# Kernel tuning notes

Hardware: AMD Instinct MI355X
Metric: run time of the kernel (lower is better)

The kernel has to match this reference:

```python
import jax, jax.numpy as jnp
import numpy as np

D = 128   # node feature dim
C = 2     # classes
N = 50000 # nodes
E = 500000  # edges (before self-loops)
H1 = 2    # conv1 heads
NEG_SLOPE = 0.2
BN_EPS = 1e-5


def setup_inputs() -> dict:
    key = jax.random.key(0)
    ks = jax.random.split(key, 24)
    rn = lambda k, shape, s=0.05: jax.random.normal(k, shape, dtype=jnp.float32) * s
    inp = {
        'x': jax.random.normal(ks[0], (N, D), dtype=jnp.float32),
        'edge_index': jax.random.randint(ks[1], (2, E), 0, N, dtype=jnp.int64),
        # conv1: GATConv(D, D, heads=2, concat=True)
        'W1': rn(ks[2], (D, H1 * D)),
        'att_src1': rn(ks[3], (H1, D)),
        'att_dst1': rn(ks[4], (H1, D)),
        'bias1': jnp.zeros((H1 * D,), jnp.float32),
        # conv2: GATConv(2D, D, heads=1, concat=False)
        'W2': rn(ks[5], (2 * D, D)),
        'att_src2': rn(ks[6], (1, D)),
        'att_dst2': rn(ks[7], (1, D)),
        'bias2': jnp.zeros((D,), jnp.float32),
        # lin1 = MLP([3D, 96]) : Linear -> ReLU -> BatchNorm1d
        'Wl': rn(ks[8], (3 * D, 96)), 'bl': jnp.zeros((96,), jnp.float32),
        'gl': jnp.ones((96,), jnp.float32), 'betal': jnp.zeros((96,), jnp.float32),
        # mlp1 = MLP([96, 96, C]) : two (Linear -> ReLU -> BN) blocks
        'Wa': rn(ks[9], (96, 96)), 'ba': jnp.zeros((96,), jnp.float32),
        'ga': jnp.ones((96,), jnp.float32), 'betaa': jnp.zeros((96,), jnp.float32),
        'Wb': rn(ks[10], (96, C)), 'bb': jnp.zeros((C,), jnp.float32),
        'gb': jnp.ones((C,), jnp.float32), 'betab': jnp.zeros((C,), jnp.float32),
    }
    return inp


def gat_conv(x, src, dst, W, att_src, att_dst, bias, heads, out_dim, concat):
    # PyG GATConv: h = x W -> [N,H,F]; per-edge logit leakyrelu(a_s.h_src + a_d.h_dst);
    # segment softmax over edges grouped by destination; weighted scatter-sum.
    n = x.shape[0]
    h = (x @ W).reshape(n, heads, out_dim)
    a_src = jnp.einsum('nhd,hd->nh', h, att_src)  # [N,H]
    a_dst = jnp.einsum('nhd,hd->nh', h, att_dst)
    alpha = jax.nn.leaky_relu(a_src[src] + a_dst[dst], NEG_SLOPE)  # [Etot,H]
    m = jax.ops.segment_max(alpha, dst, num_segments=n)            # [N,H]
    e = jnp.exp(alpha - m[dst])
    s = jax.ops.segment_sum(e, dst, num_segments=n)
    w = e / (s[dst] + 1e-16)                                       # [Etot,H]
    out = jax.ops.segment_sum(h[src] * w[:, :, None], dst, num_segments=n)  # [N,H,F]
    out = out.reshape(n, heads * out_dim) if concat else out.mean(axis=1)
    return out + bias


def mlp_block(x, W, b, gamma, beta):
    # Linear -> ReLU -> BatchNorm1d (training-mode batch stats, biased var)
    y = jax.nn.relu(x @ W + b)
    mu = y.mean(axis=0)
    var = ((y - mu) ** 2).mean(axis=0)
    return gamma * (y - mu) / jnp.sqrt(var + BN_EPS) + beta


def reference(x, edge_index, W1, att_src1, att_dst1, bias1,
              W2, att_src2, att_dst2, bias2,
              Wl, bl, gl, betal, Wa, ba, ga, betaa, Wb, bb, gb, betab):
    n = x.shape[0]
    # PyG GATConv default add_self_loops=True
    loops = jnp.arange(n, dtype=edge_index.dtype)
    src = jnp.concatenate([edge_index[0], loops])
    dst = jnp.concatenate([edge_index[1], loops])
    x1 = gat_conv(x, src, dst, W1, att_src1, att_dst1, bias1, H1, D, True)    # [N,2D]
    x2 = gat_conv(x1, src, dst, W2, att_src2, att_dst2, bias2, 1, D, False)   # [N,D]
    h = jnp.concatenate([x1, x2], axis=1)                                      # [N,3D]
    h = mlp_block(h, Wl, bl, gl, betal)     # lin1
    h = mlp_block(h, Wa, ba, ga, betaa)     # mlp1 layer 1
    h = mlp_block(h, Wb, bb, gb, betab)     # mlp1 layer 2
    return h
```

## Files before the change

kernel.cpp:

```cpp
#include <hip/hip_runtime.h>
#include <hip/hip_bf16.h>
#include <cstdint>
#include <cstddef>

#define NNODES 50000
#define NEDGES 500000
#define ETOT   (NEDGES + NNODES)

typedef __attribute__((ext_vector_type(8))) short short8;
typedef __attribute__((ext_vector_type(8))) unsigned short ushort8v;
typedef __attribute__((ext_vector_type(4))) float floatx4;
typedef __attribute__((ext_vector_type(4))) unsigned short ushort4v;

__device__ __forceinline__ unsigned short f2bf(float f) {
    union { __hip_bfloat16 h; unsigned short u; } cv;
    cv.h = __float2bfloat16(f);
    return cv.u;
}
__device__ __forceinline__ float bf2f(unsigned short u) {
    union { unsigned int i; float f; } cv;
    cv.i = ((unsigned int)u) << 16;
    return cv.f;
}

#define GBM 128
#define GBN 64
#define GBK 32

__global__ __launch_bounds__(256, 4) void gemm_mfma(
    const unsigned short* __restrict__ A, int lda,
    const unsigned short* __restrict__ Bt,
    float* __restrict__ C,
    unsigned short* __restrict__ Cb, int ldc,
    const float* __restrict__ bias,
    float* __restrict__ colsum, float* __restrict__ colsq,
    const float* __restrict__ att_s, const float* __restrict__ att_d,
    float* __restrict__ as_out, float* __restrict__ ad_out, int Hheads,
    int M, int N, int K, int do_relu)
{
    __shared__ __attribute__((aligned(16))) unsigned short Alds[GBM * GBK];
    __shared__ __attribute__((aligned(16))) unsigned short Blds[GBN * GBK];
    __shared__ float scol[GBN], sqcol[GBN];

    int tid = threadIdx.x;
    int wave = tid >> 6, lane = tid & 63;
    int row0 = blockIdx.y * GBM;
    int col0 = blockIdx.x * GBN;
    int m = lane & 15, q = lane >> 4;

    floatx4 acc[2][4] = {};

    for (int k0 = 0; k0 < K; k0 += GBK) {
        #pragma unroll
        for (int i = 0; i < 2; ++i) {
            int c = tid + i * 256;
            int r = c >> 2, off = (c & 3) * 8;
            int gr = row0 + r;
            short8 v = {};
            if (gr < M) v = *(const short8*)(A + (size_t)gr * lda + k0 + off);
            *(short8*)(Alds + r * GBK + off) = v;
        }
        {
            int r = tid >> 2, off = (tid & 3) * 8;
            short8 v = *(const short8*)(Bt + (size_t)(col0 + r) * K + k0 + off);
            *(short8*)(Blds + r * GBK + off) = v;
        }
        __syncthreads();

        short8 a0 = *(const short8*)(Alds + (wave * 32 + m) * GBK + q * 8);
        short8 a1 = *(const short8*)(Alds + (wave * 32 + 16 + m) * GBK + q * 8);
        #pragma unroll
        for (int ct = 0; ct < 4; ++ct) {
            short8 b = *(const short8*)(Blds + (ct * 16 + m) * GBK + q * 8);
            acc[0][ct] = __builtin_amdgcn_mfma_f32_16x16x32_bf16(a0, b, acc[0][ct], 0, 0, 0);
            acc[1][ct] = __builtin_amdgcn_mfma_f32_16x16x32_bf16(a1, b, acc[1][ct], 0, 0, 0);
        }
        __syncthreads();
    }

    float ps[4] = {}, pq[4] = {};
    #pragma unroll
    for (int rt = 0; rt < 2; ++rt) {
        #pragma unroll
        for (int r = 0; r < 4; ++r) {
            int gr = row0 + wave * 32 + rt * 16 + q * 4 + r;
            float ds = 0.f, dd = 0.f;
            #pragma unroll
            for (int ct = 0; ct < 4; ++ct) {
                int gc = col0 + ct * 16 + m;
                float v = acc[rt][ct][r];
                if (gc < N) {
                    float vb = v;
                    if (bias != nullptr) vb += bias[gc];
                    if (do_relu) vb = fmaxf(vb, 0.f);
                    if (att_s != nullptr) { ds += vb * att_s[gc]; dd += vb * att_d[gc]; }
                    if (gr < M) {
                        if (C  != nullptr) C[(size_t)gr * ldc + gc] = vb;
                        if (Cb != nullptr) Cb[(size_t)gr * ldc + gc] = f2bf(vb);
                        ps[ct] += vb; pq[ct] += vb * vb;
                    }
                }
            }
            if (att_s != nullptr) {
                #pragma unroll
                for (int off = 1; off < 16; off <<= 1) {
                    ds += __shfl_xor(ds, off);
                    dd += __shfl_xor(dd, off);
                }
                if (m == 0 && gr < M) {
                    int head = col0 >> 7;
                    atomicAdd(&as_out[gr * Hheads + head], ds);
                    atomicAdd(&ad_out[gr * Hheads + head], dd);
                }
            }
        }
    }
    if (colsum != nullptr) {
        if (tid < GBN) { scol[tid] = 0.f; sqcol[tid] = 0.f; }
        __syncthreads();
        #pragma unroll
        for (int ct = 0; ct < 4; ++ct) {
            atomicAdd(&scol[ct * 16 + m], ps[ct]);
            atomicAdd(&sqcol[ct * 16 + m], pq[ct]);
        }
        __syncthreads();
        if (tid < GBN) {
            int gc = col0 + tid;
            if (gc < N) {
                atomicAdd(&colsum[gc], scol[tid]);
                atomicAdd(&colsq[gc], sqcol[tid]);
            }
        }
    }
}

__global__ __launch_bounds__(256) void fold_att(
    const float* __restrict__ W1, const float* __restrict__ as1v, const float* __restrict__ ad1v,
    const float* __restrict__ W2, const float* __restrict__ as2v, const float* __restrict__ ad2v,
    float* __restrict__ U1, float* __restrict__ U2)
{
    int g = threadIdx.x >> 5, l = threadIdx.x & 31;
    int task = blockIdx.x * 8 + g;
    float ss = 0.f, sd = 0.f;
    if (task < 256) {
        int d = task & 127, h = task >> 7;
        const float4 wv = *(const float4*)(W1 + d * 256 + h * 128 + l * 4);
        const float4 av = *(const float4*)(as1v + h * 128 + l * 4);
        const float4 bv = *(const float4*)(ad1v + h * 128 + l * 4);
        ss = wv.x * av.x + wv.y * av.y + wv.z * av.z + wv.w * av.w;
        sd = wv.x * bv.x + wv.y * bv.y + wv.z * bv.z + wv.w * bv.w;
    } else {
        int k = task - 256;
        const float4 wv = *(const float4*)(W2 + (size_t)k * 128 + l * 4);
        const float4 av = *(const float4*)(as2v + l * 4);
        const float4 bv = *(const float4*)(ad2v + l * 4);
        ss = wv.x * av.x + wv.y * av.y + wv.z * av.z + wv.w * av.w;
        sd = wv.x * bv.x + wv.y * bv.y + wv.z * bv.z + wv.w * bv.w;
    }
    #pragma unroll
    for (int off = 1; off < 32; off <<= 1) { ss += __shfl_xor(ss, off); sd += __shfl_xor(sd, off); }
    if (l == 0) {
        if (task < 256) {
            int d = task & 127, h = task >> 7;
            U1[h * 128 + d] = ss;
            U1[256 + h * 128 + d] = sd;
        } else {
            int k = task - 256;
            U2[k] = ss;
            U2[256 + k] = sd;
        }
    }
}

__global__ __launch_bounds__(256) void cast_x_att(
    const float* __restrict__ x, const float* __restrict__ U1,
    unsigned short* __restrict__ xb, float* __restrict__ as1, float* __restrict__ ad1)
{
    __shared__ float Us[512];
    int tid = threadIdx.x;
    Us[tid] = U1[tid];
    Us[tid + 256] = U1[tid + 256];
    __syncthreads();
    int g = tid >> 5, l = tid & 31;
    int n = blockIdx.x * 8 + g;
    if (n >= NNODES) return;
    const float4 v = *(const float4*)(x + (size_t)n * 128 + l * 4);
    ushort4v o;
    o.x = f2bf(v.x); o.y = f2bf(v.y); o.z = f2bf(v.z); o.w = f2bf(v.w);
    *(ushort4v*)(xb + (size_t)n * 128 + l * 4) = o;
    const float4 us0 = *(const float4*)(Us + l * 4);
    const float4 us1 = *(const float4*)(Us + 128 + l * 4);
    const float4 ud0 = *(const float4*)(Us + 256 + l * 4);
    const float4 ud1 = *(const float4*)(Us + 384 + l * 4);
    float s0 = v.x * us0.x + v.y * us0.y + v.z * us0.z + v.w * us0.w;
    float s1 = v.x * us1.x + v.y * us1.y + v.z * us1.z + v.w * us1.w;
    float d0 = v.x * ud0.x + v.y * ud0.y + v.z * ud0.z + v.w * ud0.w;
    float d1 = v.x * ud1.x + v.y * ud1.y + v.z * ud1.z + v.w * ud1.w;
    #pragma unroll
    for (int off = 1; off < 32; off <<= 1) {
        s0 += __shfl_xor(s0, off); s1 += __shfl_xor(s1, off);
        d0 += __shfl_xor(d0, off); d1 += __shfl_xor(d1, off);
    }
    if (l == 0) {
        as1[n * 2] = s0; as1[n * 2 + 1] = s1;
        ad1[n * 2] = d0; ad1[n * 2 + 1] = d1;
    }
}

__global__ void cast_weights(const float* __restrict__ W1, const float* __restrict__ W2,
                             const float* __restrict__ Wl,
                             unsigned short* __restrict__ W1t, unsigned short* __restrict__ W2t,
                             unsigned short* __restrict__ Wlt) {
    int i = blockIdx.x * 256 + threadIdx.x;
    if (i < 32768) {
        int n = i >> 7, k = i & 127;
        W1t[i] = f2bf(W1[k * 256 + n]);
    } else if (i < 65536) {
        int j = i - 32768;
        int n = j >> 8, k = j & 255;
        W2t[j] = f2bf(W2[k * 128 + n]);
    } else if (i < 114688) {
        int j = i - 65536;
        int n = j / 384, k = j % 384;
        Wlt[j] = (n < 96) ? f2bf(Wl[(size_t)k * 96 + n]) : (unsigned short)0;
    }
}

__global__ void bnfold_a(const float* __restrict__ csum, const float* __restrict__ csq,
                         const float* __restrict__ gamma, const float* __restrict__ beta,
                         const float* __restrict__ Wa, const float* __restrict__ ba,
                         unsigned short* __restrict__ Wat2, float* __restrict__ ba_f) {
    __shared__ float scl[96], shf[96];
    int tid = threadIdx.x;
    if (tid < 96) {
        float mu  = csum[tid] / (float)NNODES;
        float var = csq[tid] / (float)NNODES - mu * mu;
        if (var < 0.f) var = 0.f;
        float sc = gamma[tid] * rsqrtf(var + 1e-5f);
        scl[tid] = sc; shf[tid] = beta[tid] - mu * sc;
    }
    __syncthreads();
    for (int idx = tid; idx < 128 * 96; idx += 256) {
        int n = idx / 96, k = idx % 96;
        Wat2[idx] = (n < 96) ? f2bf(scl[k] * Wa[k * 96 + n]) : (unsigned short)0;
    }
    if (tid < 96) {
        float s = ba[tid];
        for (int k = 0; k < 96; ++k) s += shf[k] * Wa[k * 96 + tid];
        ba_f[tid] = s;
    }
}

__global__ void bnfold_b(const float* __restrict__ csum, const float* __restrict__ csq,
                         const float* __restrict__ gamma, const float* __restrict__ beta,
                         const float* __restrict__ Wb, const float* __restrict__ bb,
                         unsigned short* __restrict__ Wbt, float* __restrict__ bb_f) {
    __shared__ float scl[96], shf[96];
    int tid = threadIdx.x;
    if (tid < 96) {
        float mu  = csum[tid] / (float)NNODES;
        float var = csq[tid] / (float)NNODES - mu * mu;
        if (var < 0.f) var = 0.f;
        float sc = gamma[tid] * rsqrtf(var + 1e-5f);
        scl[tid] = sc; shf[tid] = beta[tid] - mu * sc;
    }
    __syncthreads();
    for (int idx = tid; idx < 64 * 96; idx += 256) {
        int n = idx / 96, k = idx % 96;
        Wbt[idx] = (n < 2) ? f2bf(scl[k] * Wb[k * 2 + n]) : (unsigned short)0;
    }
    if (tid < 2) {
        float s = bb[tid];
        for (int k = 0; k < 96; ++k) s += shf[k] * Wb[k * 2 + tid];
        bb_f[tid] = s;
    }
}

__global__ void bn_fin_apply(const float* __restrict__ csum, const float* __restrict__ csq,
                             const float* __restrict__ gamma, const float* __restrict__ beta,
                             float* __restrict__ y, int total) {
    int i = blockIdx.x * blockDim.x + threadIdx.x;
    if (i >= total) return;
    int j = i & 1;
    float mu  = csum[j] / (float)NNODES;
    float var = csq[j] / (float)NNODES - mu * mu;
    if (var < 0.f) var = 0.f;
    float sc = gamma[j] * rsqrtf(var + 1e-5f);
    float sh = beta[j] - mu * sc;
    y[i] = y[i] * sc + sh;
}

__device__ __forceinline__ void edge_src_dst(const int* ei, int e, int& src, int& dst) {
    if (e < NEDGES) { src = ei[e]; dst = ei[NEDGES + e]; }
    else { src = e - NEDGES; dst = src; }
}

__global__ __launch_bounds__(256) void csr_count(const int* __restrict__ ei, int* __restrict__ cnt) {
    int e = blockIdx.x * blockDim.x + threadIdx.x;
    if (e >= ETOT) return;
    int src, dst; edge_src_dst(ei, e, src, dst); (void)src;
    atomicAdd(&cnt[dst], 1);
}

#define SCAN_CH 1024
#define SCAN_NB ((NNODES + SCAN_CH - 1) / SCAN_CH)

__global__ __launch_bounds__(256) void scan1(const int* __restrict__ cnt, int* __restrict__ part) {
    int t = threadIdx.x;
    int base = blockIdx.x * SCAN_CH + t * 4;
    int4 v = {0, 0, 0, 0};
    if (base + 3 < NNODES) v = *(const int4*)(cnt + base);
    else {
        if (base + 0 < NNODES) v.x = cnt[base + 0];
        if (base + 1 < NNODES) v.y = cnt[base + 1];
        if (base + 2 < NNODES) v.z = cnt[base + 2];
        if (base + 3 < NNODES) v.w = cnt[base + 3];
    }
    int s = v.x + v.y + v.z + v.w;
    __shared__ int sm[256];
    sm[t] = s;
    __syncthreads();
    for (int off = 128; off > 0; off >>= 1) {
        if (t < off) sm[t] += sm[t + off];
        __syncthreads();
    }
    if (t == 0) part[blockIdx.x] = sm[0];
}

__global__ void scan2(int* __restrict__ part, int* __restrict__ rowstart) {
    int lane = threadIdx.x;
    int v = (lane < SCAN_NB) ? part[lane] : 0;
    #pragma unroll
    for (int off = 1; off < 64; off <<= 1) {
        int t = __shfl_up(v, off);
        if (lane >= off) v += t;
    }
    int ex = __shfl_up(v, 1);
    if (lane == 0) ex = 0;
    if (lane < SCAN_NB) part[lane] = ex;
    if (lane == 0) rowstart[NNODES] = ETOT;
}

__global__ __launch_bounds__(256) void scan3(const int* __restrict__ cnt, const int* __restrict__ part,
                                             int* __restrict__ rowstart, int* __restrict__ cursor) {
    int t = threadIdx.x;
    int base = blockIdx.x * SCAN_CH + t * 4;
    int4 v = {0, 0, 0, 0};
    if (base + 3 < NNODES) v = *(const int4*)(cnt + base);
    else {
        if (base + 0 < NNODES) v.x = cnt[base + 0];
        if (base + 1 < NNODES) v.y = cnt[base + 1];
        if (base + 2 < NNODES) v.z = cnt[base + 2];
        if (base + 3 < NNODES) v.w = cnt[base + 3];
    }
    int s = v.x + v.y + v.z + v.w;
    __shared__ int sm[2][256];
    sm[0][t] = s;
    __syncthreads();
    int cur = 0;
    #pragma unroll
    for (int off = 1; off < 256; off <<= 1) {
        int nxt = cur ^ 1;
        int val = sm[cur][t];
        if (t >= off) val += sm[cur][t - off];
        sm[nxt][t] = val;
        __syncthreads();
        cur = nxt;
    }
    int p = sm[cur][t] - s + part[blockIdx.x];
    if (base + 0 < NNODES) { rowstart[base + 0] = p; cursor[base + 0] = p; } p += v.x;
    if (base + 1 < NNODES) { rowstart[base + 1] = p; cursor[base + 1] = p; } p += v.y;
    if (base + 2 < NNODES) { rowstart[base + 2] = p; cursor[base + 2] = p; } p += v.z;
    if (base + 3 < NNODES) { rowstart[base + 3] = p; cursor[base + 3] = p; }
}

__global__ __launch_bounds__(256) void csr_fill(const int* __restrict__ ei,
                                                int* __restrict__ cursor,
                                                int* __restrict__ esrc) {
    int e = blockIdx.x * blockDim.x + threadIdx.x;
    if (e >= ETOT) return;
    int src, dst; edge_src_dst(ei, e, src, dst);
    int pos = atomicAdd(&cursor[dst], 1);
    esrc[pos] = src;
}

__global__ __launch_bounds__(256) void gat_gather_x2(
    const int* __restrict__ rowstart, const int* __restrict__ esrc,
    const unsigned short* __restrict__ xb, const float* __restrict__ a_src,
    const float* __restrict__ a_dst, unsigned short* __restrict__ xaggh)
{
    int tid = threadIdx.x;
    int t = tid & 15;
    int g0 = (blockIdx.x * blockDim.x + tid) >> 4;
    int gstride = (gridDim.x * blockDim.x) >> 4;

    for (int n = g0; n < NNODES; n += gstride) {
        int beg = rowstart[n], deg = rowstart[n + 1] - beg;
        const float2 adv = *(const float2*)(a_dst + (size_t)n * 2);
        float acc0[8] = {}, acc1[8] = {};

        if (deg <= 32) {
            int sa = 0, sb = 0;
            float la0 = -1e30f, la1 = -1e30f;
            float lb0 = -1e30f, lb1 = -1e30f;
            if (t < deg) {
                sa = esrc[beg + t];
                const float2 asv = *(const float2*)(a_src + (size_t)sa * 2);
                la0 = asv.x + adv.x; la0 = la0 >= 0.f ? la0 : 0.2f * la0;
                lb0 = asv.y + adv.y; lb0 = lb0 >= 0.f ? lb0 : 0.2f * lb0;
            }
            if (t + 16 < deg) {
                sb = esrc[beg + 16 + t];
                const float2 asv = *(const float2*)(a_src + (size_t)sb * 2);
                la1 = asv.x + adv.x; la1 = la1 >= 0.f ? la1 : 0.2f * la1;
                lb1 = asv.y + adv.y; lb1 = lb1 >= 0.f ? lb1 : 0.2f * lb1;
            }
            float m0 = fmaxf(la0, la1), m1 = fmaxf(lb0, lb1);
            #pragma unroll
            for (int off = 1; off < 16; off <<= 1) {
                m0 = fmaxf(m0, __shfl_xor(m0, off, 16));
                m1 = fmaxf(m1, __shfl_xor(m1, off, 16));
            }
            float ea0 = (t < deg)      ? __expf(la0 - m0) : 0.f;
            float ea1 = (t + 16 < deg) ? __expf(la1 - m0) : 0.f;
            float eb0 = (t < deg)      ? __expf(lb0 - m1) : 0.f;
            float eb1 = (t + 16 < deg) ? __expf(lb1 - m1) : 0.f;
            float s0 = ea0 + ea1, s1 = eb0 + eb1;
            #pragma unroll
            for (int off = 1; off < 16; off <<= 1) {
                s0 += __shfl_xor(s0, off, 16);
                s1 += __shfl_xor(s1, off, 16);
            }
            float i0 = 1.f / (s0 + 1e-16f), i1 = 1.f / (s1 + 1e-16f);
            float wa0 = ea0 * i0, wa1 = ea1 * i0;
            float wb0 = eb0 * i1, wb1 = eb1 * i1;

            int e = 0;
            for (; e + 3 < deg; e += 4) {
                int sx[4]; float w0x[4], w1x[4];
                #pragma unroll
                for (int u = 0; u < 4; ++u) {
                    int ee = e + u;
                    int hi = ee & 16, ln = ee & 15;
                    sx[u]  = __shfl(hi ? sb  : sa,  ln, 16);
                    w0x[u] = __shfl(hi ? wa1 : wa0, ln, 16);
                    w1x[u] = __shfl(hi ? wb1 : wb0, ln, 16);
                }
                ushort8v hv[4];
                #pragma unroll
                for (int u = 0; u < 4; ++u)
                    hv[u] = *(const ushort8v*)(xb + (size_t)sx[u] * 128 + t * 8);
                #pragma unroll
                for (int u = 0; u < 4; ++u) {
                    #pragma unroll
                    for (int j = 0; j < 8; ++j) {
                        float f = bf2f(hv[u][j]);
                        acc0[j] += w0x[u] * f;
                        acc1[j] += w1x[u] * f;
                    }
                }
            }
            for (; e < deg; ++e) {
                int hi = e & 16, ln = e & 15;
                int   sX  = __shfl(hi ? sb  : sa,  ln, 16);
                float wX0 = __shfl(hi ? wa1 : wa0, ln, 16);
                float wX1 = __shfl(hi ? wb1 : wb0, ln, 16);
                const ushort8v hv = *(const ushort8v*)(xb + (size_t)sX * 128 + t * 8);
                #pragma unroll
                for (int j = 0; j < 8; ++j) {
                    float f = bf2f(hv[j]);
                    acc0[j] += wX0 * f; acc1[j] += wX1 * f;
                }
            }
        } else {
            float m0 = -1e30f, m1 = -1e30f;
            for (int idx = t; idx < deg; idx += 16) {
                int s = esrc[beg + idx];
                const float2 asv = *(const float2*)(a_src + (size_t)s * 2);
                float l0 = asv.x + adv.x; l0 = l0 >= 0.f ? l0 : 0.2f * l0;
                float l1 = asv.y + adv.y; l1 = l1 >= 0.f ? l1 : 0.2f * l1;
                m0 = fmaxf(m0, l0); m1 = fmaxf(m1, l1);
            }
            #pragma unroll
            for (int off = 1; off < 16; off <<= 1) {
                m0 = fmaxf(m0, __shfl_xor(m0, off, 16));
                m1 = fmaxf(m1, __shfl_xor(m1, off, 16));
            }
            float s0 = 0.f, s1 = 0.f;
            for (int idx = t; idx < deg; idx += 16) {
                int s = esrc[beg + idx];
                const float2 asv = *(const float2*)(a_src + (size_t)s * 2);
                float l0 = asv.x + adv.x; l0 = l0 >= 0.f ? l0 : 0.2f * l0;
                float l1 = asv.y + adv.y; l1 = l1 >= 0.f ? l1 : 0.2f * l1;
                s0 += __expf(l0 - m0); s1 += __expf(l1 - m1);
            }
            #pragma unroll
            for (int off = 1; off < 16; off <<= 1) {
                s0 += __shfl_xor(s0, off, 16);
                s1 += __shfl_xor(s1, off, 16);
            }
            float inv0 = 1.f / (s0 + 1e-16f), inv1 = 1.f / (s1 + 1e-16f);
            for (int e = 0; e < deg; ++e) {
                int s = esrc[beg + e];
                const float2 asv = *(const float2*)(a_src + (size_t)s * 2);
                float l0 = asv.x + adv.x; l0 = l0 >= 0.f ? l0 : 0.2f * l0;
                float l1 = asv.y + adv.y; l1 = l1 >= 0.f ? l1 : 0.2f * l1;
                float w0 = __expf(l0 - m0) * inv0, w1 = __expf(l1 - m1) * inv1;
                const ushort8v hv = *(const ushort8v*)(xb + (size_t)s * 128 + t * 8);
                #pragma unroll
                for (int j = 0; j < 8; ++j) {
                    float f = bf2f(hv[j]);
                    acc0[j] += w0 * f; acc1[j] += w1 * f;
                }
            }
        }

        ushort8v o0, o1;
        #pragma unroll
        for (int j = 0; j < 8; ++j) { o0[j] = f2bf(acc0[j]); o1[j] = f2bf(acc1[j]); }
        *(ushort8v*)(xaggh + (size_t)n * 256 + t * 8) = o0;
        *(ushort8v*)(xaggh + (size_t)n * 256 + 128 + t * 8) = o1;
    }
}

__global__ __launch_bounds__(256) void gat_gather_h1(
    const int* __restrict__ rowstart, const int* __restrict__ esrc,
    const unsigned short* __restrict__ hb, const float* __restrict__ a_src,
    const float* __restrict__ a_dst, const float* __restrict__ bias,
    unsigned short* __restrict__ xcat)
{
    int tid = threadIdx.x;
    int t = tid & 15;
    int g0 = (blockIdx.x * blockDim.x + tid) >> 4;
    int gstride = (gridDim.x * blockDim.x) >> 4;

    for (int n = g0; n < NNODES; n += gstride) {
        int beg = rowstart[n], deg = rowstart[n + 1] - beg;
        float ad0 = a_dst[n];
        float acc[8] = {};

        if (deg <= 32) {
            int sa = 0, sb = 0;
            float l0 = -1e30f, l1 = -1e30f;
            if (t < deg) {
                sa = esrc[beg + t];
                l0 = a_src[sa] + ad0; l0 = l0 >= 0.f ? l0 : 0.2f * l0;
            }
            if (t + 16 < deg) {
                sb = esrc[beg + 16 + t];
                l1 = a_src[sb] + ad0; l1 = l1 >= 0.f ? l1 : 0.2f * l1;
            }
            float m0 = fmaxf(l0, l1);
            #pragma unroll
            for (int off = 1; off < 16; off <<= 1)
                m0 = fmaxf(m0, __shfl_xor(m0, off, 16));
            float e0 = (t < deg)      ? __expf(l0 - m0) : 0.f;
            float e1 = (t + 16 < deg) ? __expf(l1 - m0) : 0.f;
            float s0 = e0 + e1;
            #pragma unroll
            for (int off = 1; off < 16; off <<= 1)
                s0 += __shfl_xor(s0, off, 16);
            float i0 = 1.f / (s0 + 1e-16f);
            float w0 = e0 * i0, w1 = e1 * i0;

            int e = 0;
            for (; e + 3 < deg; e += 4) {
                int sx[4]; float wx[4];
                #pragma unroll
                for (int u = 0; u < 4; ++u) {
                    int ee = e + u;
                    int hi = ee & 16, ln = ee & 15;
                    sx[u] = __shfl(hi ? sb : sa, ln, 16);
                    wx[u] = __shfl(hi ? w1 : w0, ln, 16);
                }
                ushort8v hv[4];
                #pragma unroll
                for (int u = 0; u < 4; ++u)
                    hv[u] = *(const ushort8v*)(hb + (size_t)sx[u] * 128 + t * 8);
                #pragma unroll
                for (int u = 0; u < 4; ++u) {
                    #pragma unroll
                    for (int j = 0; j < 8; ++j)
                        acc[j] += wx[u] * bf2f(hv[u][j]);
                }
            }
            for (; e < deg; ++e) {
                int hi = e & 16, ln = e & 15;
                int   sX = __shfl(hi ? sb : sa, ln, 16);
                float wX = __shfl(hi ? w1 : w0, ln, 16);
                const ushort8v hv = *(const ushort8v*)(hb + (size_t)sX * 128 + t * 8);
                #pragma unroll
                for (int j = 0; j < 8; ++j) acc[j] += wX * bf2f(hv[j]);
            }
        } else {
            float m0 = -1e30f;
            for (int idx = t; idx < deg; idx += 16) {
                int s = esrc[beg + idx];
                float l = a_src[s] + ad0; l = l >= 0.f ? l : 0.2f * l;
                m0 = fmaxf(m0, l);
            }
            #pragma unroll
            for (int off = 1; off < 16; off <<= 1)
                m0 = fmaxf(m0, __shfl_xor(m0, off, 16));
            float s0 = 0.f;
            for (int idx = t; idx < deg; idx += 16) {
                int s = esrc[beg + idx];
                float l = a_src[s] + ad0; l = l >= 0.f ? l : 0.2f * l;
                s0 += __expf(l - m0);
            }
            #pragma unroll
            for (int off = 1; off < 16; off <<= 1)
                s0 += __shfl_xor(s0, off, 16);
            float inv0 = 1.f / (s0 + 1e-16f);
            for (int e = 0; e < deg; ++e) {
                int s = esrc[beg + e];
                float l = a_src[s] + ad0; l = l >= 0.f ? l : 0.2f * l;
                float w = __expf(l - m0) * inv0;
                const ushort8v hv = *(const ushort8v*)(hb + (size_t)s * 128 + t * 8);
                #pragma unroll
                for (int j = 0; j < 8; ++j) acc[j] += w * bf2f(hv[j]);
            }
        }

        const float4 b0 = *(const float4*)(bias + t * 8);
        const float4 b1 = *(const float4*)(bias + t * 8 + 4);
        ushort8v o;
        o[0] = f2bf(acc[0] + b0.x); o[1] = f2bf(acc[1] + b0.y);
        o[2] = f2bf(acc[2] + b0.z); o[3] = f2bf(acc[3] + b0.w);
        o[4] = f2bf(acc[4] + b1.x); o[5] = f2bf(acc[5] + b1.y);
        o[6] = f2bf(acc[6] + b1.z); o[7] = f2bf(acc[7] + b1.w);
        *(ushort8v*)(xcat + (size_t)n * 384 + 256 + t * 8) = o;
    }
}

extern "C" void kernel_launch(void* const* d_in, const int* in_sizes, int n_in,
                              void* d_out, int out_size, void* d_ws, size_t ws_size,
                              hipStream_t stream) {
    const float* x        = (const float*)d_in[0];
    const int*   ei       = (const int*)d_in[1];
    const float* W1       = (const float*)d_in[2];
    const float* att_src1 = (const float*)d_in[3];
    const float* att_dst1 = (const float*)d_in[4];
    const float* bias1    = (const float*)d_in[5];
    const float* W2       = (const float*)d_in[6];
    const float* att_src2 = (const float*)d_in[7];
    const float* att_dst2 = (const float*)d_in[8];
    const float* bias2    = (const float*)d_in[9];
    const float* Wl       = (const float*)d_in[10];
    const float* bl       = (const float*)d_in[11];
    const float* gl       = (const float*)d_in[12];
    const float* betal    = (const float*)d_in[13];
    const float* Wa       = (const float*)d_in[14];
    const float* ba       = (const float*)d_in[15];
    const float* ga       = (const float*)d_in[16];
    const float* betaa    = (const float*)d_in[17];
    const float* Wb       = (const float*)d_in[18];
    const float* bb       = (const float*)d_in[19];
    const float* gb       = (const float*)d_in[20];
    const float* betab    = (const float*)d_in[21];
    float* out = (float*)d_out;
    char* ws = (char*)d_ws;

    const int N = NNODES;

    const size_t offY2b  = 0;
    const size_t offXcat = 19200000;
    const size_t offXb   = 57600000;
    const size_t offY1b  = 70400000;
    const size_t offXagg = 80000000;
    const size_t offW1t  = 105600000;
    const size_t offW2t  = 105665536;
    const size_t offWlt  = 105731072;
    const size_t offWat2 = 105829376;
    const size_t offWbt  = 105853952;
    const size_t offBaf  = 105866240;
    const size_t offBbf  = 105866640;
    const size_t offU1   = 105867264;
    const size_t offU2   = 105869312;
    const size_t offRow  = 106000000;
    const size_t offCur  = 106200128;
    const size_t offEsrc = 106400832;
    const size_t offPart = 108700000;
    const size_t offAs1  = 108800000;
    const size_t offAd1  = 109200000;
    const size_t offAs2  = 109600000;
    const size_t offAd2  = 109800000;
    const size_t offSt   = 110000000;

    unsigned short* y2b   = (unsigned short*)(ws + offY2b);
    unsigned short* xcat  = (unsigned short*)(ws + offXcat);
    unsigned short* xb    = (unsigned short*)(ws + offXb);
    unsigned short* hb2   = (unsigned short*)(ws + offXb);
    unsigned short* y1b   = (unsigned short*)(ws + offY1b);
    unsigned short* xaggh = (unsigned short*)(ws + offXagg);
    unsigned short* W1t   = (unsigned short*)(ws + offW1t);
    unsigned short* W2t   = (unsigned short*)(ws + offW2t);
    unsigned short* Wlt   = (unsigned short*)(ws + offWlt);
    unsigned short* Wat2  = (unsigned short*)(ws + offWat2);
    unsigned short* Wbt   = (unsigned short*)(ws + offWbt);
    float* ba_f = (float*)(ws + offBaf);
    float* bb_f = (float*)(ws + offBbf);
    float* U1   = (float*)(ws + offU1);
    float* U2   = (float*)(ws + offU2);
    int* rowst  = (int*)(ws + offRow);
    int* cursor = (int*)(ws + offCur);
    int* esrc   = (int*)(ws + offEsrc);
    int* part   = (int*)(ws + offPart);
    float* as1  = (float*)(ws + offAs1);
    float* ad1  = (float*)(ws + offAd1);
    float* as2  = (float*)(ws + offAs2);
    float* ad2  = (float*)(ws + offAd2);

    float* csum_l = (float*)(ws + offSt + 0);
    float* csq_l  = (float*)(ws + offSt + 512);
    float* csum_a = (float*)(ws + offSt + 2048);
    float* csq_a  = (float*)(ws + offSt + 2560);
    float* csum_b = (float*)(ws + offSt + 4096);
    float* csq_b  = (float*)(ws + offSt + 4608);

    hipMemsetAsync(ws + offRow, 0, (NNODES + 1) * sizeof(int), stream);
    hipMemsetAsync(ws + offAs1, 0, (offSt + 6144) - offAs1, stream);

    dim3 blk(256);
    int edgeBlocks = (ETOT + 255) / 256;
    int gatherBlocks = 2048;
    dim3 gemmRows((N + GBM - 1) / GBM);

    fold_att<<<64, blk, 0, stream>>>(W1, att_src1, att_dst1, W2, att_src2, att_dst2, U1, U2);
    cast_x_att<<<(N + 7) / 8, blk, 0, stream>>>(x, U1, xb, as1, ad1);
    cast_weights<<<(114688 + 255) / 256, blk, 0, stream>>>(W1, W2, Wl, W1t, W2t, Wlt);

    csr_count<<<edgeBlocks, blk, 0, stream>>>(ei, rowst);
    scan1<<<SCAN_NB, blk, 0, stream>>>(rowst, part);
    scan2<<<1, 64, 0, stream>>>(part, rowst);
    scan3<<<SCAN_NB, blk, 0, stream>>>(rowst, part, rowst, cursor);
    csr_fill<<<edgeBlocks, blk, 0, stream>>>(ei, cursor, esrc);

    gat_gather_x2<<<gatherBlocks, blk, 0, stream>>>(rowst, esrc, xb, as1, ad1, xaggh);
    gemm_mfma<<<dim3(2, gemmRows.x), blk, 0, stream>>>(
        xaggh, 256, W1t, nullptr, xcat, 384, bias1, nullptr, nullptr,
        U2, U2 + 256, as2, ad2, 1, N, 128, 128, 0);
    gemm_mfma<<<dim3(2, gemmRows.x), blk, 0, stream>>>(
        xaggh + 128, 256, W1t + 128 * 128, nullptr, xcat + 128, 384, bias1 + 128,
        nullptr, nullptr, U2 + 128, U2 + 384, as2, ad2, 1, N, 128, 128, 0);

    gemm_mfma<<<dim3(2, gemmRows.x), blk, 0, stream>>>(
        xcat, 384, W2t, nullptr, hb2, 128, nullptr, nullptr, nullptr,
        nullptr, nullptr, nullptr, nullptr, 0, N, 128, 256, 0);
    gat_gather_h1<<<gatherBlocks, blk, 0, stream>>>(rowst, esrc, hb2, as2, ad2, bias2, xcat);

    gemm_mfma<<<dim3(2, gemmRows.x), blk, 0, stream>>>(
        xcat, 384, Wlt, nullptr, y1b, 96, bl, csum_l, csq_l,
        nullptr, nullptr, nullptr, nullptr, 0, N, 96, 384, 1);
    bnfold_a<<<1, 256, 0, stream>>>(csum_l, csq_l, gl, betal, Wa, ba, Wat2, ba_f);

    gemm_mfma<<<dim3(2, gemmRows.x), blk, 0, stream>>>(
        y1b, 96, Wat2, nullptr, y2b, 96, ba_f, csum_a, csq_a,
        nullptr, nullptr, nullptr, nullptr, 0, N, 96, 96, 1);
    bnfold_b<<<1, 256, 0, stream>>>(csum_a, csq_a, ga, betaa, Wb, bb, Wbt, bb_f);

    gemm_mfma<<<dim3(1, gemmRows.x), blk, 0, stream>>>(
        y2b, 96, Wbt, out, nullptr, 2, bb_f, csum_b, csq_b,
        nullptr, nullptr, nullptr, nullptr, 0, N, 2, 96, 1);

    bn_fin_apply<<<(N * 2 + 255) / 256, blk, 0, stream>>>(csum_b, csq_b, gb, betab, out, N * 2);
}
```

Before: 383.9 us.

## Fuse conv1 gather with W1 projection and merge small setup kernels

The layer-1 attention gather now writes each 16-node tile of aggregated features to shared memory and immediately multiplies it by W1 with MFMA. The same kernel adds bias, emits the bf16 output and accumulates the layer-2 attention logits. This removes the intermediate xaggh round trip through global memory and two GEMM launches. Weight casting is merged into the attention-fold kernel, and the scan2/scan3 kernels are merged so each block recomputes the partial prefix itself. In exchange, the fused kernel gives up the grid-stride loop and reads W1t straight from global/L2 in every block instead of staging it in shared memory.

Measured after the change: 349.1 us. 9.1% less time.

```diff
diff --git a/kernel.cpp b/kernel.cpp
--- a/kernel.cpp
+++ b/kernel.cpp
@@ -34,8 +34,6 @@
     unsigned short* __restrict__ Cb, int ldc,
     const float* __restrict__ bias,
     float* __restrict__ colsum, float* __restrict__ colsq,
-    const float* __restrict__ att_s, const float* __restrict__ att_d,
-    float* __restrict__ as_out, float* __restrict__ ad_out, int Hheads,
     int M, int N, int K, int do_relu)
 {
     __shared__ __attribute__((aligned(16))) unsigned short Alds[GBM * GBK];
@@ -84,7 +82,6 @@
         #pragma unroll
         for (int r = 0; r < 4; ++r) {
             int gr = row0 + wave * 32 + rt * 16 + q * 4 + r;
-            float ds = 0.f, dd = 0.f;
             #pragma unroll
             for (int ct = 0; ct < 4; ++ct) {
                 int gc = col0 + ct * 16 + m;
@@ -93,7 +90,6 @@
                     float vb = v;
                     if (bias != nullptr) vb += bias[gc];
                     if (do_relu) vb = fmaxf(vb, 0.f);
-                    if (att_s != nullptr) { ds += vb * att_s[gc]; dd += vb * att_d[gc]; }
                     if (gr < M) {
                         if (C  != nullptr) C[(size_t)gr * ldc + gc] = vb;
                         if (Cb != nullptr) Cb[(size_t)gr * ldc + gc] = f2bf(vb);
@@ -101,18 +97,6 @@
                     }
                 }
             }
-            if (att_s != nullptr) {
-                #pragma unroll
-                for (int off = 1; off < 16; off <<= 1) {
-                    ds += __shfl_xor(ds, off);
-                    dd += __shfl_xor(dd, off);
-                }
-                if (m == 0 && gr < M) {
-                    int head = col0 >> 7;
-                    atomicAdd(&as_out[gr * Hheads + head], ds);
-                    atomicAdd(&ad_out[gr * Hheads + head], dd);
-                }
-            }
         }
     }
     if (colsum != nullptr) {
@@ -134,40 +118,59 @@
     }
 }
 
-__global__ __launch_bounds__(256) void fold_att(
+__global__ __launch_bounds__(256) void fold_cast(
     const float* __restrict__ W1, const float* __restrict__ as1v, const float* __restrict__ ad1v,
     const float* __restrict__ W2, const float* __restrict__ as2v, const float* __restrict__ ad2v,
-    float* __restrict__ U1, float* __restrict__ U2)
+    const float* __restrict__ Wl,
+    float* __restrict__ U1, float* __restrict__ U2,
+    unsigned short* __restrict__ W1t, unsigned short* __restrict__ W2t,
+    unsigned short* __restrict__ Wlt)
 {
-    int g = threadIdx.x >> 5, l = threadIdx.x & 31;
-    int task = blockIdx.x * 8 + g;
-    float ss = 0.f, sd = 0.f;
-    if (task < 256) {
-        int d = task & 127, h = task >> 7;
-        const float4 wv = *(const float4*)(W1 + d * 256 + h * 128 + l * 4);
-        const float4 av = *(const float4*)(as1v + h * 128 + l * 4);
-        const float4 bv = *(const float4*)(ad1v + h * 128 + l * 4);
-        ss = wv.x * av.x + wv.y * av.y + wv.z * av.z + wv.w * av.w;
-        sd = wv.x * bv.x + wv.y * bv.y + wv.z * bv.z + wv.w * bv.w;
-    } else {
-        int k = task - 256;
-        const float4 wv = *(const float4*)(W2 + (size_t)k * 128 + l * 4);
-        const float4 av = *(const float4*)(as2v + l * 4);
-        const float4 bv = *(const float4*)(ad2v + l * 4);
-        ss = wv.x * av.x + wv.y * av.y + wv.z * av.z + wv.w * av.w;
-        sd = wv.x * bv.x + wv.y * bv.y + wv.z * bv.z + wv.w * bv.w;
-    }
-    #pragma unroll
-    for (int off = 1; off < 32; off <<= 1) { ss += __shfl_xor(ss, off); sd += __shfl_xor(sd, off); }
-    if (l == 0) {
+    if (blockIdx.x < 64) {
+        int g = threadIdx.x >> 5, l = threadIdx.x & 31;
+        int task = blockIdx.x * 8 + g;
+        float ss = 0.f, sd = 0.f;
         if (task < 256) {
             int d = task & 127, h = task >> 7;
-            U1[h * 128 + d] = ss;
-            U1[256 + h * 128 + d] = sd;
+            const float4 wv = *(const float4*)(W1 + d * 256 + h * 128 + l * 4);
+            const float4 av = *(const float4*)(as1v + h * 128 + l * 4);
+            const float4 bv = *(const float4*)(ad1v + h * 128 + l * 4);
+            ss = wv.x * av.x + wv.y * av.y + wv.z * av.z + wv.w * av.w;
+            sd = wv.x * bv.x + wv.y * bv.y + wv.z * bv.z + wv.w * bv.w;
         } else {
             int k = task - 256;
-            U2[k] = ss;
-            U2[256 + k] = sd;
+            const float4 wv = *(const float4*)(W2 + (size_t)k * 128 + l * 4);
+            const float4 av = *(const float4*)(as2v + l * 4);
+            const float4 bv = *(const float4*)(ad2v + l * 4);
+            ss = wv.x * av.x + wv.y * av.y + wv.z * av.z + wv.w * av.w;
+            sd = wv.x * bv.x + wv.y * bv.y + wv.z * bv.z + wv.w * bv.w;
+        }
+        #pragma unroll
+        for (int off = 1; off < 32; off <<= 1) { ss += __shfl_xor(ss, off); sd += __shfl_xor(sd, off); }
+        if (l == 0) {
+            if (task < 256) {
+                int d = task & 127, h = task >> 7;
+                U1[h * 128 + d] = ss;
+                U1[256 + h * 128 + d] = sd;
+            } else {
+                int k = task - 256;
+                U2[k] = ss;
+                U2[256 + k] = sd;
+            }
+        }
+    } else {
+        int i = (blockIdx.x - 64) * 256 + threadIdx.x;
+        if (i < 32768) {
+            int n = i >> 7, k = i & 127;
+            W1t[i] = f2bf(W1[k * 256 + n]);
+        } else if (i < 65536) {
+            int j = i - 32768;
+            int n = j >> 8, k = j & 255;
+            W2t[j] = f2bf(W2[k * 128 + n]);
+        } else if (i < 114688) {
+            int j = i - 65536;
+            int n = j / 384, k = j % 384;
+            Wlt[j] = (n < 96) ? f2bf(Wl[(size_t)k * 96 + n]) : (unsigned short)0;
         }
     }
 }
@@ -207,25 +210,6 @@
     }
 }
 
-__global__ void cast_weights(const float* __restrict__ W1, const float* __restrict__ W2,
-                             const float* __restrict__ Wl,
-                             unsigned short* __restrict__ W1t, unsigned short* __restrict__ W2t,
-                             unsigned short* __restrict__ Wlt) {
-    int i = blockIdx.x * 256 + threadIdx.x;
-    if (i < 32768) {
-        int n = i >> 7, k = i & 127;
-        W1t[i] = f2bf(W1[k * 256 + n]);
-    } else if (i < 65536) {
-        int j = i - 32768;
-        int n = j >> 8, k = j & 255;
-        W2t[j] = f2bf(W2[k * 128 + n]);
-    } else if (i < 114688) {
-        int j = i - 65536;
-        int n = j / 384, k = j % 384;
-        Wlt[j] = (n < 96) ? f2bf(Wl[(size_t)k * 96 + n]) : (unsigned short)0;
-    }
-}
-
 __global__ void bnfold_a(const float* __restrict__ csum, const float* __restrict__ csq,
                          const float* __restrict__ gamma, const float* __restrict__ beta,
                          const float* __restrict__ Wa, const float* __restrict__ ba,
@@ -327,23 +311,22 @@
     if (t == 0) part[blockIdx.x] = sm[0];
 }
 
-__global__ void scan2(int* __restrict__ part, int* __restrict__ rowstart) {
-    int lane = threadIdx.x;
-    int v = (lane < SCAN_NB) ? part[lane] : 0;
-    #pragma unroll
-    for (int off = 1; off < 64; off <<= 1) {
-        int t = __shfl_up(v, off);
-        if (lane >= off) v += t;
-    }
-    int ex = __shfl_up(v, 1);
-    if (lane == 0) ex = 0;
-    if (lane < SCAN_NB) part[lane] = ex;
-    if (lane == 0) rowstart[NNODES] = ETOT;
-}
-
-__global__ __launch_bounds__(256) void scan3(const int* __restrict__ cnt, const int* __restrict__ part,
-                                             int* __restrict__ rowstart, int* __restrict__ cursor) {
+__global__ __launch_bounds__(256) void scan23(const int* __restrict__ cnt, const int* __restrict__ part,
+                                              int* __restrict__ rowstart, int* __restrict__ cursor) {
+    __shared__ int sbase;
     int t = threadIdx.x;
+    if (t < 64) {
+        int v = (t < SCAN_NB) ? part[t] : 0;
+        #pragma unroll
+        for (int off = 1; off < 64; off <<= 1) {
+            int u = __shfl_up(v, off);
+            if (t >= off) v += u;
+        }
+        int ex = __shfl_up(v, 1);
+        if (t == 0) ex = 0;
+        if (t == (int)blockIdx.x) sbase = ex;
+        if (blockIdx.x == 0 && t == 0) rowstart[NNODES] = ETOT;
+    }
     int base = blockIdx.x * SCAN_CH + t * 4;
     int4 v = {0, 0, 0, 0};
     if (base + 3 < NNODES) v = *(const int4*)(cnt + base);
@@ -367,7 +350,7 @@
         __syncthreads();
         cur = nxt;
     }
-    int p = sm[cur][t] - s + part[blockIdx.x];
+    int p = sm[cur][t] - s + sbase;
     if (base + 0 < NNODES) { rowstart[base + 0] = p; cursor[base + 0] = p; } p += v.x;
     if (base + 1 < NNODES) { rowstart[base + 1] = p; cursor[base + 1] = p; } p += v.y;
     if (base + 2 < NNODES) { rowstart[base + 2] = p; cursor[base + 2] = p; } p += v.z;
@@ -384,142 +367,194 @@
     esrc[pos] = src;
 }
 
-__global__ __launch_bounds__(256) void gat_gather_x2(
+__global__ __launch_bounds__(256, 4) void gat_conv1_fused(
     const int* __restrict__ rowstart, const int* __restrict__ esrc,
     const unsigned short* __restrict__ xb, const float* __restrict__ a_src,
-    const float* __restrict__ a_dst, unsigned short* __restrict__ xaggh)
+    const float* __restrict__ a_dst, const unsigned short* __restrict__ W1t,
+    const float* __restrict__ bias1, const float* __restrict__ U2,
+    unsigned short* __restrict__ xcat, float* __restrict__ as2, float* __restrict__ ad2)
 {
+    __shared__ __attribute__((aligned(16))) unsigned short Alds[16 * 264];
+    __shared__ float U2s[512];
+    __shared__ float Bs[256];
+
     int tid = threadIdx.x;
     int t = tid & 15;
-    int g0 = (blockIdx.x * blockDim.x + tid) >> 4;
-    int gstride = (gridDim.x * blockDim.x) >> 4;
-
-    for (int n = g0; n < NNODES; n += gstride) {
-        int beg = rowstart[n], deg = rowstart[n + 1] - beg;
-        const float2 adv = *(const float2*)(a_dst + (size_t)n * 2);
-        float acc0[8] = {}, acc1[8] = {};
-
-        if (deg <= 32) {
-            int sa = 0, sb = 0;
-            float la0 = -1e30f, la1 = -1e30f;
-            float lb0 = -1e30f, lb1 = -1e30f;
-            if (t < deg) {
-                sa = esrc[beg + t];
-                const float2 asv = *(const float2*)(a_src + (size_t)sa * 2);
-                la0 = asv.x + adv.x; la0 = la0 >= 0.f ? la0 : 0.2f * la0;
-                lb0 = asv.y + adv.y; lb0 = lb0 >= 0.f ? lb0 : 0.2f * lb0;
-            }
-            if (t + 16 < deg) {
-                sb = esrc[beg + 16 + t];
-                const float2 asv = *(const float2*)(a_src + (size_t)sb * 2);
-                la1 = asv.x + adv.x; la1 = la1 >= 0.f ? la1 : 0.2f * la1;
-                lb1 = asv.y + adv.y; lb1 = lb1 >= 0.f ? lb1 : 0.2f * lb1;
-            }
-            float m0 = fmaxf(la0, la1), m1 = fmaxf(lb0, lb1);
-            #pragma unroll
-            for (int off = 1; off < 16; off <<= 1) {
-                m0 = fmaxf(m0, __shfl_xor(m0, off, 16));
-                m1 = fmaxf(m1, __shfl_xor(m1, off, 16));
-            }
-            float ea0 = (t < deg)      ? __expf(la0 - m0) : 0.f;
-            float ea1 = (t + 16 < deg) ? __expf(la1 - m0) : 0.f;
-            float eb0 = (t < deg)      ? __expf(lb0 - m1) : 0.f;
-            float eb1 = (t + 16 < deg) ? __expf(lb1 - m1) : 0.f;
-            float s0 = ea0 + ea1, s1 = eb0 + eb1;
-            #pragma unroll
-            for (int off = 1; off < 16; off <<= 1) {
-                s0 += __shfl_xor(s0, off, 16);
-                s1 += __shfl_xor(s1, off, 16);
-            }
-            float i0 = 1.f / (s0 + 1e-16f), i1 = 1.f / (s1 + 1e-16f);
-            float wa0 = ea0 * i0, wa1 = ea1 * i0;
-            float wb0 = eb0 * i1, wb1 = eb1 * i1;
-
-            int e = 0;
-            for (; e + 3 < deg; e += 4) {
-                int sx[4]; float w0x[4], w1x[4];
-                #pragma unroll
-                for (int u = 0; u < 4; ++u) {
-                    int ee = e + u;
-                    int hi = ee & 16, ln = ee & 15;
-                    sx[u]  = __shfl(hi ? sb  : sa,  ln, 16);
-                    w0x[u] = __shfl(hi ? wa1 : wa0, ln, 16);
-                    w1x[u] = __shfl(hi ? wb1 : wb0, ln, 16);
-                }
-                ushort8v hv[4];
-                #pragma unroll
-                for (int u = 0; u < 4; ++u)
-                    hv[u] = *(const ushort8v*)(xb + (size_t)sx[u] * 128 + t * 8);
-                #pragma unroll
-                for (int u = 0; u < 4; ++u) {
-                    #pragma unroll
-                    for (int j = 0; j < 8; ++j) {
-                        float f = bf2f(hv[u][j]);
-                        acc0[j] += w0x[u] * f;
-                        acc1[j] += w1x[u] * f;
-                    }
-                }
-            }
-            for (; e < deg; ++e) {
-                int hi = e & 16, ln = e & 15;
-                int   sX  = __shfl(hi ? sb  : sa,  ln, 16);
-                float wX0 = __shfl(hi ? wa1 : wa0, ln, 16);
-                float wX1 = __shfl(hi ? wb1 : wb0, ln, 16);
-                const ushort8v hv = *(const ushort8v*)(xb + (size_t)sX * 128 + t * 8);
+    int g = tid >> 4;
+    int nb = blockIdx.x * 16;
+    int n = nb + g;
+
+    U2s[tid] = U2[tid];
+    U2s[tid + 256] = U2[tid + 256];
+    Bs[tid] = bias1[tid];
+
+    int beg = rowstart[n], deg = rowstart[n + 1] - beg;
+    const float2 adv = *(const float2*)(a_dst + (size_t)n * 2);
+    float acc0[8] = {}, acc1[8] = {};
+
+    if (deg <= 32) {
+        int sa = 0, sb = 0;
+        float la0 = -1e30f, la1 = -1e30f;
+        float lb0 = -1e30f, lb1 = -1e30f;
+        if (t < deg) {
+            sa = esrc[beg + t];
+            const float2 asv = *(const float2*)(a_src + (size_t)sa * 2);
+            la0 = asv.x + adv.x; la0 = la0 >= 0.f ? la0 : 0.2f * la0;
+            lb0 = asv.y + adv.y; lb0 = lb0 >= 0.f ? lb0 : 0.2f * lb0;
+        }
+        if (t + 16 < deg) {
+            sb = esrc[beg + 16 + t];
+            const float2 asv = *(const float2*)(a_src + (size_t)sb * 2);
+            la1 = asv.x + adv.x; la1 = la1 >= 0.f ? la1 : 0.2f * la1;
+            lb1 = asv.y + adv.y; lb1 = lb1 >= 0.f ? lb1 : 0.2f * lb1;
+        }
+        float m0 = fmaxf(la0, la1), m1 = fmaxf(lb0, lb1);
+        #pragma unroll
+        for (int off = 1; off < 16; off <<= 1) {
+            m0 = fmaxf(m0, __shfl_xor(m0, off, 16));
+            m1 = fmaxf(m1, __shfl_xor(m1, off, 16));
+        }
+        float ea0 = (t < deg)      ? __expf(la0 - m0) : 0.f;
+        float ea1 = (t + 16 < deg) ? __expf(la1 - m0) : 0.f;
+        float eb0 = (t < deg)      ? __expf(lb0 - m1) : 0.f;
+        float eb1 = (t + 16 < deg) ? __expf(lb1 - m1) : 0.f;
+        float s0 = ea0 + ea1, s1 = eb0 + eb1;
+        #pragma unroll
+        for (int off = 1; off < 16; off <<= 1) {
+            s0 += __shfl_xor(s0, off, 16);
+            s1 += __shfl_xor(s1, off, 16);
+        }
+        float i0 = 1.f / (s0 + 1e-16f), i1 = 1.f / (s1 + 1e-16f);
+        float wa0 = ea0 * i0, wa1 = ea1 * i0;
+        float wb0 = eb0 * i1, wb1 = eb1 * i1;
+
+        int e = 0;
+        for (; e + 3 < deg; e += 4) {
+            int sx[4]; float w0x[4], w1x[4];
+            #pragma unroll
+            for (int u = 0; u < 4; ++u) {
+                int ee = e + u;
+                int hi = ee & 16, ln = ee & 15;
+                sx[u]  = __shfl(hi ? sb  : sa,  ln, 16);
+                w0x[u] = __shfl(hi ? wa1 : wa0, ln, 16);
+                w1x[u] = __shfl(hi ? wb1 : wb0, ln, 16);
+            }
+            ushort8v hv[4];
+            #pragma unroll
+            for (int u = 0; u < 4; ++u)
+                hv[u] = *(const ushort8v*)(xb + (size_t)sx[u] * 128 + t * 8);
+            #pragma unroll
+            for (int u = 0; u < 4; ++u) {
                 #pragma unroll
                 for (int j = 0; j < 8; ++j) {
-                    float f = bf2f(hv[j]);
-                    acc0[j] += wX0 * f; acc1[j] += wX1 * f;
+                    float f = bf2f(hv[u][j]);
+                    acc0[j] += w0x[u] * f;
+                    acc1[j] += w1x[u] * f;
                 }
             }
-        } else {
-            float m0 = -1e30f, m1 = -1e30f;
-            for (int idx = t; idx < deg; idx += 16) {
-                int s = esrc[beg + idx];
-                const float2 asv = *(const float2*)(a_src + (size_t)s * 2);
-                float l0 = asv.x + adv.x; l0 = l0 >= 0.f ? l0 : 0.2f * l0;
-                float l1 = asv.y + adv.y; l1 = l1 >= 0.f ? l1 : 0.2f * l1;
-                m0 = fmaxf(m0, l0); m1 = fmaxf(m1, l1);
-            }
-            #pragma unroll
-            for (int off = 1; off < 16; off <<= 1) {
-                m0 = fmaxf(m0, __shfl_xor(m0, off, 16));
-                m1 = fmaxf(m1, __shfl_xor(m1, off, 16));
-            }
-            float s0 = 0.f, s1 = 0.f;
-            for (int idx = t; idx < deg; idx += 16) {
-                int s = esrc[beg + idx];
-                const float2 asv = *(const float2*)(a_src + (size_t)s * 2);
-                float l0 = asv.x + adv.x; l0 = l0 >= 0.f ? l0 : 0.2f * l0;
-                float l1 = asv.y + adv.y; l1 = l1 >= 0.f ? l1 : 0.2f * l1;
-                s0 += __expf(l0 - m0); s1 += __expf(l1 - m1);
-            }
-            #pragma unroll
-            for (int off = 1; off < 16; off <<= 1) {
-                s0 += __shfl_xor(s0, off, 16);
-                s1 += __shfl_xor(s1, off, 16);
-            }
-            float inv0 = 1.f / (s0 + 1e-16f), inv1 = 1.f / (s1 + 1e-16f);
-            for (int e = 0; e < deg; ++e) {
-                int s = esrc[beg + e];
-                const float2 asv = *(const float2*)(a_src + (size_t)s * 2);
-                float l0 = asv.x + adv.x; l0 = l0 >= 0.f ? l0 : 0.2f * l0;
-                float l1 = asv.y + adv.y; l1 = l1 >= 0.f ? l1 : 0.2f * l1;
-                float w0 = __expf(l0 - m0) * inv0, w1 = __expf(l1 - m1) * inv1;
-                const ushort8v hv = *(const ushort8v*)(xb + (size_t)s * 128 + t * 8);
-                #pragma unroll
-                for (int j = 0; j < 8; ++j) {
-                    float f = bf2f(hv[j]);
-                    acc0[j] += w0 * f; acc1[j] += w1 * f;
-                }
-            }
-        }
-
+        }
+        for (; e < deg; ++e) {
+            int hi = e & 16, ln = e & 15;
+            int   sX  = __shfl(hi ? sb  : sa,  ln, 16);
+            float wX0 = __shfl(hi ? wa1 : wa0, ln, 16);
+            float wX1 = __shfl(hi ? wb1 : wb0, ln, 16);
+            const ushort8v hv = *(const ushort8v*)(xb + (size_t)sX * 128 + t * 8);
+            #pragma unroll
+            for (int j = 0; j < 8; ++j) {
+                float f = bf2f(hv[j]);
+                acc0[j] += wX0 * f; acc1[j] += wX1 * f;
+            }
+        }
+    } else {
+        float m0 = -1e30f, m1 = -1e30f;
+        for (int idx = t; idx < deg; idx += 16) {
+            int s = esrc[beg + idx];
+            const float2 asv = *(const float2*)(a_src + (size_t)s * 2);
+            float l0 = asv.x + adv.x; l0 = l0 >= 0.f ? l0 : 0.2f * l0;
+            float l1 = asv.y + adv.y; l1 = l1 >= 0.f ? l1 : 0.2f * l1;
+            m0 = fmaxf(m0, l0); m1 = fmaxf(m1, l1);
+        }
+        #pragma unroll
+        for (int off = 1; off < 16; off <<= 1) {
+            m0 = fmaxf(m0, __shfl_xor(m0, off, 16));
+            m1 = fmaxf(m1, __shfl_xor(m1, off, 16));
+        }
+        float s0 = 0.f, s1 = 0.f;
+        for (int idx = t; idx < deg; idx += 16) {
+            int s = esrc[beg + idx];
+            const float2 asv = *(const float2*)(a_src + (size_t)s * 2);
+            float l0 = asv.x + adv.x; l0 = l0 >= 0.f ? l0 : 0.2f * l0;
+            float l1 = asv.y + adv.y; l1 = l1 >= 0.f ? l1 : 0.2f * l1;
+            s0 += __expf(l0 - m0); s1 += __expf(l1 - m1);
+        }
+        #pragma unroll
+        for (int off = 1; off < 16; off <<= 1) {
+            s0 += __shfl_xor(s0, off, 16);
+            s1 += __shfl_xor(s1, off, 16);
+        }
+        float inv0 = 1.f / (s0 + 1e-16f), inv1 = 1.f / (s1 + 1e-16f);
+        for (int e = 0; e < deg; ++e) {
+            int s = esrc[beg + e];
+            const float2 asv = *(const float2*)(a_src + (size_t)s * 2);
+            float l0 = asv.x + adv.x; l0 = l0 >= 0.f ? l0 : 0.2f * l0;
+            float l1 = asv.y + adv.y; l1 = l1 >= 0.f ? l1 : 0.2f * l1;
+            float w0 = __expf(l0 - m0) * inv0, w1 = __expf(l1 - m1) * inv1;
+            const ushort8v hv = *(const ushort8v*)(xb + (size_t)s * 128 + t * 8);
+            #pragma unroll
+            for (int j = 0; j < 8; ++j) {
+                float f = bf2f(hv[j]);
+                acc0[j] += w0 * f; acc1[j] += w1 * f;
+            }
+        }
+    }
+
+    {
         ushort8v o0, o1;
         #pragma unroll
         for (int j = 0; j < 8; ++j) { o0[j] = f2bf(acc0[j]); o1[j] = f2bf(acc1[j]); }
-        *(ushort8v*)(xaggh + (size_t)n * 256 + t * 8) = o0;
-        *(ushort8v*)(xaggh + (size_t)n * 256 + 128 + t * 8) = o1;
+        *(ushort8v*)(Alds + g * 264 + t * 8) = o0;
+        *(ushort8v*)(Alds + g * 264 + 128 + t * 8) = o1;
+    }
+    __syncthreads();
+
+    int wave = tid >> 6, lane = tid & 63;
+    int m = lane & 15, q = lane >> 4;
+    int ncol0 = wave * 64;
+    int kbase = (wave >= 2) ? 128 : 0;
+
+    floatx4 cacc[4] = {};
+    #pragma unroll
+    for (int ks = 0; ks < 4; ++ks) {
+        short8 a = *(const short8*)(Alds + m * 264 + kbase + ks * 32 + q * 8);
+        #pragma unroll
+        for (int ct = 0; ct < 4; ++ct) {
+            short8 b = *(const short8*)(W1t + (size_t)(ncol0 + ct * 16 + m) * 128 + ks * 32 + q * 8);
+            cacc[ct] = __builtin_amdgcn_mfma_f32_16x16x32_bf16(a, b, cacc[ct], 0, 0, 0);
+        }
+    }
+
+    #pragma unroll
+    for (int r = 0; r < 4; ++r) {
+        int row = q * 4 + r;
+        int gn = nb + row;
+        float ds = 0.f, dd = 0.f;
+        #pragma unroll
+        for (int ct = 0; ct < 4; ++ct) {
+            int col = ncol0 + ct * 16 + m;
+            float vb = cacc[ct][r] + Bs[col];
+            ds += vb * U2s[col];
+            dd += vb * U2s[256 + col];
+            xcat[(size_t)gn * 384 + col] = f2bf(vb);
+        }
+        #pragma unroll
+        for (int off = 1; off < 16; off <<= 1) {
+            ds += __shfl_xor(ds, off);
+            dd += __shfl_xor(dd, off);
+        }
+        if (m == 0) {
+            atomicAdd(&as2[gn], ds);
+            atomicAdd(&ad2[gn], dd);
+        }
     }
 }
 
@@ -667,7 +702,6 @@
     const size_t offXcat = 19200000;
     const size_t offXb   = 57600000;
     const size_t offY1b  = 70400000;
-    const size_t offXagg = 80000000;
     const size_t offW1t  = 105600000;
     const size_t offW2t  = 105665536;
     const size_t offWlt  = 105731072;
@@ -692,7 +726,6 @@
     unsigned short* xb    = (unsigned short*)(ws + offXb);
     unsigned short* hb2   = (unsigned short*)(ws + offXb);
     unsigned short* y1b   = (unsigned short*)(ws + offY1b);
-    unsigned short* xaggh = (unsigned short*)(ws + offXagg);
     unsigned short* W1t   = (unsigned short*)(ws + offW1t);
     unsigned short* W2t   = (unsigned short*)(ws + offW2t);
     unsigned short* Wlt   = (unsigned short*)(ws + offWlt);
@@ -726,42 +759,36 @@
     int gatherBlocks = 2048;
     dim3 gemmRows((N + GBM - 1) / GBM);
 
-    fold_att<<<64, blk, 0, stream>>>(W1, att_src1, att_dst1, W2, att_src2, att_dst2, U1, U2);
+    fold_cast<<<512, blk, 0, stream>>>(W1, att_src1, att_dst1, W2, att_src2, att_dst2,
+                                       Wl, U1, U2, W1t, W2t, Wlt);
     cast_x_att<<<(N + 7) / 8, blk, 0, stream>>>(x, U1, xb, as1, ad1);
-    cast_weights<<<(114688 + 255) / 256, blk, 0, stream>>>(W1, W2, Wl, W1t, W2t, Wlt);
 
     csr_count<<<edgeBlocks, blk, 0, stream>>>(ei, rowst);
     scan1<<<SCAN_NB, blk, 0, stream>>>(rowst, part);
-    scan2<<<1, 64, 0, stream>>>(part, rowst);
-    scan3<<<SCAN_NB, blk, 0, stream>>>(rowst, part, rowst, cursor);
+    scan23<<<SCAN_NB, blk, 0, stream>>>(rowst, part, rowst, cursor);
     csr_fill<<<edgeBlocks, blk, 0, stream>>>(ei, cursor, esrc);
 
-    gat_gather_x2<<<gatherBlocks, blk, 0, stream>>>(rowst, esrc, xb, as1, ad1, xaggh);
-    gemm_mfma<<<dim3(2, gemmRows.x), blk, 0, stream>>>(
-        xaggh, 256, W1t, nullptr, xcat, 384, bias1, nullptr, nullptr,
-        U2, U2 + 256, as2, ad2, 1, N, 128, 128, 0);
-    gemm_mfma<<<dim3(2, gemmRows.x), blk, 0, stream>>>(
-        xaggh + 128, 256, W1t + 128 * 128, nullptr, xcat + 128, 384, bias1 + 128,
-        nullptr, nullptr, U2 + 128, U2 + 384, as2, ad2, 1, N, 128, 128, 0);
+    gat_conv1_fused<<<NNODES / 16, blk, 0, stream>>>(
+        rowst, esrc, xb, as1, ad1, W1t, bias1, U2, xcat, as2, ad2);
 
     gemm_mfma<<<dim3(2, gemmRows.x), blk, 0, stream>>>(
         xcat, 384, W2t, nullptr, hb2, 128, nullptr, nullptr, nullptr,
-        nullptr, nullptr, nullptr, nullptr, 0, N, 128, 256, 0);
+        N, 128, 256, 0);
     gat_gather_h1<<<gatherBlocks, blk, 0, stream>>>(rowst, esrc, hb2, as2, ad2, bias2, xcat);
 
     gemm_mfma<<<dim3(2, gemmRows.x), blk, 0, stream>>>(
         xcat, 384, Wlt, nullptr, y1b, 96, bl, csum_l, csq_l,
-        nullptr, nullptr, nullptr, nullptr, 0, N, 96, 384, 1);
+        N, 96, 384, 1);
     bnfold_a<<<1, 256, 0, stream>>>(csum_l, csq_l, gl, betal, Wa, ba, Wat2, ba_f);
 
     gemm_mfma<<<dim3(2, gemmRows.x), blk, 0, stream>>>(
         y1b, 96, Wat2, nullptr, y2b, 96, ba_f, csum_a, csq_a,
-        nullptr, nullptr, nullptr, nullptr, 0, N, 96, 96, 1);
+        N, 96, 96, 1);
     bnfold_b<<<1, 256, 0, stream>>>(csum_a, csq_a, ga, betaa, Wb, bb, Wbt, bb_f);
 
     gemm_mfma<<<dim3(1, gemmRows.x), blk, 0, stream>>>(
         y2b, 96, Wbt, out, nullptr, 2, bb_f, csum_b, csq_b,
-        nullptr, nullptr, nullptr, nullptr, 0, N, 2, 96, 1);
+        N, 2, 96, 1);
 
     bn_fin_apply<<<(N * 2 + 255) / 256, blk, 0, stream>>>(csum_b, csq_b, gb, betab, out, N * 2);
 }
```
